# Kernel optimization log

Hardware: AMD Instinct MI355X
Metric: run time of the kernel (lower is better)

Reference implementation:

```python
import jax, jax.numpy as jnp
import numpy as np

N = 30000
SLOPE = 0.2  # PyG GATConv default negative_slope


def _gat_conv(x, src, dst, W, a_src, a_dst, b, heads, out_ch, concat):
    """PyG GATConv (add_self_loops already applied), eval mode (no dropout).
    x: [N, F_in]; src/dst: [E] int; W: [F_in, heads*out_ch];
    a_src/a_dst: [heads, out_ch]; b: [heads*out_ch] or [out_ch]."""
    n = x.shape[0]
    h = (x @ W).reshape(n, heads, out_ch)              # [N, H, C]
    al_src = jnp.sum(h * a_src, axis=-1)               # [N, H]
    al_dst = jnp.sum(h * a_dst, axis=-1)               # [N, H]
    e = jax.nn.leaky_relu(al_src[src] + al_dst[dst], SLOPE)  # [E, H]
    # segment softmax over incoming edges of each destination node
    m = jax.ops.segment_max(e, dst, num_segments=n)
    ex = jnp.exp(e - m[dst])
    denom = jax.ops.segment_sum(ex, dst, num_segments=n)
    alpha = ex / (denom[dst] + 1e-16)                  # [E, H]
    msg = h[src] * alpha[..., None]                    # [E, H, C]
    out = jax.ops.segment_sum(msg, dst, num_segments=n)  # [N, H, C]
    out = out.reshape(n, heads * out_ch) if concat else out.mean(axis=1)
    return out + b


def setup_inputs() -> dict:
    key = jax.random.key(0)
    ks = jax.random.split(key, 20)
    E = 480000
    IN, H0, H1, LAT = 256, 64, 128, 32
    HEADS = 4
    x = jax.random.normal(ks[0], (N, IN), dtype=jnp.float32)
    edge_index = jax.random.randint(ks[1], (2, E), 0, N, dtype=jnp.int32)

    def gp(k, fin, heads, outc, concat):
        k1, k2, k3, k4 = jax.random.split(k, 4)
        s = 0.1
        W = jax.random.normal(k1, (fin, heads * outc), dtype=jnp.float32) * s
        a_s = jax.random.normal(k2, (heads, outc), dtype=jnp.float32) * s
        a_d = jax.random.normal(k3, (heads, outc), dtype=jnp.float32) * s
        b = jax.random.normal(k4, (heads * outc if concat else outc,), dtype=jnp.float32) * s
        return W, a_s, a_d, b

    W1, as1, ad1, b1 = gp(ks[2], IN, HEADS, H0, True)
    W2, as2, ad2, b2 = gp(ks[3], H0 * HEADS, HEADS, H1, True)
    Wm, asm, adm, bm = gp(ks[4], H1 * HEADS, HEADS, LAT, False)
    Wl, asl, adl, bl = gp(ks[5], H1 * HEADS, HEADS, LAT, False)
    return dict(x=x, edge_index=edge_index,
                W1=W1, as1=as1, ad1=ad1, b1=b1,
                W2=W2, as2=as2, ad2=ad2, b2=b2,
                Wm=Wm, asm=asm, adm=adm, bm=bm,
                Wl=Wl, asl=asl, adl=adl, bl=bl)


def reference(x, edge_index, W1, as1, ad1, b1, W2, as2, ad2, b2,
              Wm, asm, adm, bm, Wl, asl, adl, bl):
    n = x.shape[0]
    # add self loops (PyG GATConv default)
    loop = jnp.arange(n, dtype=edge_index.dtype)
    src = jnp.concatenate([edge_index[0], loop])
    dst = jnp.concatenate([edge_index[1], loop])

    out = _gat_conv(x, src, dst, W1, as1, ad1, b1, heads=4, out_ch=64, concat=True)
    out = jax.nn.relu(out)
    out = _gat_conv(out, src, dst, W2, as2, ad2, b2, heads=4, out_ch=128, concat=True)
    out = jax.nn.relu(out)
    # F.dropout with training=False (eval) is identity
    z_mean = _gat_conv(out, src, dst, Wm, asm, adm, bm, heads=4, out_ch=32, concat=False)
    z_logstd = _gat_conv(out, src, dst, Wl, asl, adl, bl, heads=4, out_ch=32, concat=False)
    return z_mean, z_logstd
```

## Files before the change

### kernel.cpp

```cpp
#include <hip/hip_runtime.h>
#include <cstddef>

typedef __attribute__((ext_vector_type(8))) short short8;
typedef __attribute__((ext_vector_type(4))) float f32x4;
typedef __attribute__((ext_vector_type(8))) _Float16 half8;
typedef __attribute__((ext_vector_type(4))) _Float16 half4;

__device__ __forceinline__ unsigned short f2h(float f) {
    union { _Float16 h; unsigned short u; } x; x.h = (_Float16)f; return x.u;
}
__device__ __forceinline__ float lrelu(float v) { return v > 0.f ? v : 0.2f * v; }


__global__ void count_edges_kernel(const int* __restrict__ ei, int E, int N,
                                   int* __restrict__ cnt) {
    int e = blockIdx.x * blockDim.x + threadIdx.x;
    if (e >= E + N) return;
    int d = (e < E) ? ei[E + e] : (e - E);
    atomicAdd(&cnt[d], 1);
}

__global__ void scan_kernel(int* __restrict__ cnt, int* __restrict__ rp, int n) {
    __shared__ int sh[1024];
    int t = threadIdx.x;
    int chunk = (n + 1023) >> 10;
    int beg = t * chunk;
    int end = beg + chunk < n ? beg + chunk : n;
    int local = 0;
    for (int i = beg; i < end; i++) local += cnt[i];
    sh[t] = local;
    __syncthreads();
    for (int off = 1; off < 1024; off <<= 1) {
        int v = (t >= off) ? sh[t - off] : 0;
        __syncthreads();
        sh[t] += v;
        __syncthreads();
    }
    int run = (t == 0) ? 0 : sh[t - 1];
    for (int i = beg; i < end; i++) {
        int c = cnt[i];
        cnt[i] = 0;
        run += c;
        rp[i + 1] = run;
    }
    if (t == 0) rp[0] = 0;
}

__global__ void scatter_edges_kernel(const int* __restrict__ ei, int E, int N,
                                     const int* __restrict__ rp, int* __restrict__ cur,
                                     int* __restrict__ csrc) {
    int e = blockIdx.x * blockDim.x + threadIdx.x;
    if (e >= E + N) return;
    int s, d;
    if (e < E) { s = ei[e]; d = ei[E + e]; } else { s = e - E; d = s; }
    int pos = rp[d] + atomicAdd(&cur[d], 1);
    csrc[pos] = s;
}


__global__ void f32_to_f16_pad4_kernel(const float* __restrict__ in,
                                       unsigned short* __restrict__ out,
                                       int rows, int cols, int padRows) {
    int i = blockIdx.x * blockDim.x + threadIdx.x;
    int total = (padRows * cols) >> 2;
    if (i >= total) return;
    int r = (i * 4) / cols;
    ushort4 o;
    if (r < rows) {
        float4 v = *(const float4*)(in + (size_t)i * 4);
        o = make_ushort4(f2h(v.x), f2h(v.y), f2h(v.z), f2h(v.w));
    } else {
        o = make_ushort4(0, 0, 0, 0);
    }
    *(ushort4*)(out + (size_t)i * 4) = o;
}

__global__ void transpose_all_kernel(
    const float* __restrict__ W1, const float* __restrict__ W2,
    const float* __restrict__ Wm, const float* __restrict__ Wl,
    unsigned short* __restrict__ W1t, unsigned short* __restrict__ W2t,
    unsigned short* __restrict__ WmlT) {
    int i = blockIdx.x * blockDim.x + threadIdx.x;
    if (i < 65536) {
        int k = i >> 8, n = i & 255;
        W1t[(size_t)n * 256 + k] = f2h(W1[i]);
    } else if (i < 65536 + 131072) {
        int j = i - 65536;
        int k = j >> 9, n = j & 511;
        W2t[(size_t)n * 256 + k] = f2h(W2[j]);
    } else if (i < 65536 + 131072 + 65536) {
        int j = i - 196608;
        int k = j >> 7, n = j & 127;
        WmlT[(size_t)n * 512 + k] = f2h(Wm[j]);
    } else if (i < 65536 + 131072 + 131072) {
        int j = i - 262144;
        int k = j >> 7, n = j & 127;
        WmlT[(size_t)(128 + n) * 512 + k] = f2h(Wl[j]);
    }
}


__global__ __launch_bounds__(256) void gemm_f16_kernel(
    const unsigned short* __restrict__ A, const unsigned short* __restrict__ Bt,
    unsigned short* __restrict__ C, int M, int K, int Nc,
    float* __restrict__ al_s, float* __restrict__ al_d,
    const float* __restrict__ aslo, const float* __restrict__ adlo,
    const float* __restrict__ ashi, const float* __restrict__ adhi,
    int csplit, int Chead, int H) {
    __shared__ short As[64 * 32];
    __shared__ short Bs[128 * 32];
    __shared__ float salS[64][4];
    __shared__ float salD[64][4];
    int tid = threadIdx.x;
    int bm = blockIdx.y * 64;
    int bn = blockIdx.x * 128;
    int wave = tid >> 6, lane = tid & 63;
    int wm = (wave >> 1) * 32, wn = (wave & 1) * 64;
    int lm = lane & 15, lq = lane >> 4;

    f32x4 acc[2][4] = {};

    int c0 = tid, c1 = tid + 256;
    const unsigned short* Ap0 = A + (size_t)(bm + (c0 >> 2)) * K + (c0 & 3) * 8;
    const unsigned short* Bp0 = Bt + (size_t)(bn + (c0 >> 2)) * K + (c0 & 3) * 8;
    const unsigned short* Bp1 = Bt + (size_t)(bn + (c1 >> 2)) * K + (c1 & 3) * 8;

    short8 a0 = *(const short8*)(Ap0);
    short8 b0 = *(const short8*)(Bp0);
    short8 b1 = *(const short8*)(Bp1);

    for (int kk = 0; kk < K; kk += 32) {
        __syncthreads();
        *(short8*)&As[c0 * 8] = a0;
        *(short8*)&Bs[c0 * 8] = b0;
        *(short8*)&Bs[c1 * 8] = b1;
        if (kk + 32 < K) {
            a0 = *(const short8*)(Ap0 + kk + 32);
            b0 = *(const short8*)(Bp0 + kk + 32);
            b1 = *(const short8*)(Bp1 + kk + 32);
        }
        __syncthreads();
        half8 af[2], bf[4];
#pragma unroll
        for (int t = 0; t < 2; t++)
            af[t] = *(const half8*)&As[(wm + t * 16 + lm) * 32 + lq * 8];
#pragma unroll
        for (int t = 0; t < 4; t++)
            bf[t] = *(const half8*)&Bs[(wn + t * 16 + lm) * 32 + lq * 8];
#pragma unroll
        for (int tm = 0; tm < 2; tm++)
#pragma unroll
            for (int tn = 0; tn < 4; tn++)
                acc[tm][tn] = __builtin_amdgcn_mfma_f32_16x16x32_f16(
                    af[tm], bf[tn], acc[tm][tn], 0, 0, 0);
    }

#pragma unroll
    for (int tm = 0; tm < 2; tm++) {
#pragma unroll
        for (int r = 0; r < 4; r++) {
            int row = bm + wm + tm * 16 + lq * 4 + r;
            if (row < M) {
#pragma unroll
                for (int tn = 0; tn < 4; tn++) {
                    int col = bn + wn + tn * 16 + lm;
                    C[(size_t)row * Nc + col] = f2h(acc[tm][tn][r]);
                }
            }
        }
    }

    float asv[4], adv[4];
#pragma unroll
    for (int tn = 0; tn < 4; tn++) {
        int col = bn + wn + tn * 16 + lm;
        bool hi = col >= csplit;
        int cc = hi ? col - csplit : col;
        asv[tn] = hi ? ashi[cc] : aslo[cc];
        adv[tn] = hi ? adhi[cc] : adlo[cc];
    }
    int gb = wn >> 5;
#pragma unroll
    for (int tm = 0; tm < 2; tm++) {
#pragma unroll
        for (int r = 0; r < 4; r++) {
#pragma unroll
            for (int p = 0; p < 2; p++) {
                float s1 = acc[tm][2 * p][r] * asv[2 * p]
                         + acc[tm][2 * p + 1][r] * asv[2 * p + 1];
                float s2 = acc[tm][2 * p][r] * adv[2 * p]
                         + acc[tm][2 * p + 1][r] * adv[2 * p + 1];
#pragma unroll
                for (int off = 8; off >= 1; off >>= 1) {
                    s1 += __shfl_xor(s1, off);
                    s2 += __shfl_xor(s2, off);
                }
                if (lm == 0) {
                    int rl = wm + tm * 16 + lq * 4 + r;
                    salS[rl][gb + p] = s1;
                    salD[rl][gb + p] = s2;
                }
            }
        }
    }
    __syncthreads();
    if (tid < 64) {
        int row = bm + tid;
        if (row < M) {
            int hb = bn / Chead;
            int HB = 128 / Chead;
            int GH = Chead >> 5;
            for (int i = 0; i < HB; i++) {
                float ss = 0.f, sd = 0.f;
                for (int j = 0; j < GH; j++) {
                    ss += salS[tid][i * GH + j];
                    sd += salD[tid][i * GH + j];
                }
                al_s[(size_t)row * H + hb + i] = ss;
                al_d[(size_t)row * H + hb + i] = sd;
            }
        }
    }
}


template <int H4, int V, int MODE>
__global__ __launch_bounds__(256) void gat_fused_kernel(
    const int* __restrict__ rp, const int* __restrict__ csrc,
    const float* __restrict__ al_s, const float* __restrict__ al_d,
    const unsigned short* __restrict__ h,
    const float* __restrict__ bias1, const float* __restrict__ bias2,
    void* __restrict__ out1v, void* __restrict__ out2v, int HC, int C, int N) {
    const int H = 4 * H4;
    __shared__ int lds_src[4][64];
    __shared__ float lds_alpha[4][64 * 4 * H4];
    __shared__ float shred[4][256];
    int wv = threadIdx.x >> 6;
    int lane = threadIdx.x & 63;
    int n = blockIdx.x * 4 + wv;
    if (n >= N) return;
    int beg = rp[n], end = rp[n + 1];
    int deg = end - beg;

    float ad[H];
#pragma unroll
    for (int g = 0; g < H4; g++)
        *(float4*)&ad[g * 4] = *(const float4*)(al_d + (size_t)n * H + g * 4);

    int ch = lane * V;
    int hh = ch / C;
    half8 acc8 = {};
    half4 acc4 = {};

    if (deg <= 64) {
        bool act = lane < deg;
        int s = act ? csrc[beg + lane] : 0;
        float v[H], m[H], ex[H], sum[H];
#pragma unroll
        for (int g = 0; g < H4; g++) {
            float4 as = *(const float4*)(al_s + (size_t)s * H + g * 4);
            v[g * 4 + 0] = lrelu(as.x + ad[g * 4 + 0]);
            v[g * 4 + 1] = lrelu(as.y + ad[g * 4 + 1]);
            v[g * 4 + 2] = lrelu(as.z + ad[g * 4 + 2]);
            v[g * 4 + 3] = lrelu(as.w + ad[g * 4 + 3]);
        }
#pragma unroll
        for (int j = 0; j < H; j++) m[j] = act ? v[j] : -3.402823466e38f;
#pragma unroll
        for (int off = 32; off >= 1; off >>= 1)
#pragma unroll
            for (int j = 0; j < H; j++) m[j] = fmaxf(m[j], __shfl_xor(m[j], off));
#pragma unroll
        for (int j = 0; j < H; j++) {
            ex[j] = act ? __expf(v[j] - m[j]) : 0.f;
            sum[j] = ex[j];
        }
#pragma unroll
        for (int off = 32; off >= 1; off >>= 1)
#pragma unroll
            for (int j = 0; j < H; j++) sum[j] += __shfl_xor(sum[j], off);
        if (act) {
            lds_src[wv][lane] = s;
#pragma unroll
            for (int g = 0; g < H4; g++) {
                float4 o;
                o.x = ex[g * 4 + 0] / (sum[g * 4 + 0] + 1e-16f);
                o.y = ex[g * 4 + 1] / (sum[g * 4 + 1] + 1e-16f);
                o.z = ex[g * 4 + 2] / (sum[g * 4 + 2] + 1e-16f);
                o.w = ex[g * 4 + 3] / (sum[g * 4 + 3] + 1e-16f);
                *(float4*)&lds_alpha[wv][lane * H + g * 4] = o;
            }
        }
        int t = 0;
        for (; t + 8 <= deg; t += 8) {
            int ss[8]; float av[8];
#pragma unroll
            for (int u = 0; u < 8; u++) {
                ss[u] = lds_src[wv][t + u];
                av[u] = lds_alpha[wv][(t + u) * H + hh];
            }
            if constexpr (V == 8) {
                half8 hv[8];
#pragma unroll
                for (int u = 0; u < 8; u++)
                    hv[u] = *(const half8*)(h + (size_t)ss[u] * HC + ch);
#pragma unroll
                for (int u = 0; u < 8; u++) {
                    _Float16 ah = (_Float16)av[u];
                    half8 a2;
#pragma unroll
                    for (int i = 0; i < 8; i++) a2[i] = ah;
                    acc8 += hv[u] * a2;
                }
            } else {
                half4 hv[8];
#pragma unroll
                for (int u = 0; u < 8; u++)
                    hv[u] = *(const half4*)(h + (size_t)ss[u] * HC + ch);
#pragma unroll
                for (int u = 0; u < 8; u++) {
                    _Float16 ah = (_Float16)av[u];
                    half4 a2;
#pragma unroll
                    for (int i = 0; i < 4; i++) a2[i] = ah;
                    acc4 += hv[u] * a2;
                }
            }
        }
        for (; t < deg; t++) {
            int s2 = lds_src[wv][t];
            _Float16 ah = (_Float16)lds_alpha[wv][t * H + hh];
            if constexpr (V == 8) {
                half8 hv = *(const half8*)(h + (size_t)s2 * HC + ch);
                half8 a2;
#pragma unroll
                for (int i = 0; i < 8; i++) a2[i] = ah;
                acc8 += hv * a2;
            } else {
                half4 hv = *(const half4*)(h + (size_t)s2 * HC + ch);
                half4 a2;
#pragma unroll
                for (int i = 0; i < 4; i++) a2[i] = ah;
                acc4 += hv * a2;
            }
        }
    } else {
        float m[H], sum[H];
#pragma unroll
        for (int j = 0; j < H; j++) m[j] = -3.402823466e38f;
        for (int e = beg + lane; e < end; e += 64) {
            int s = csrc[e];
#pragma unroll
            for (int g = 0; g < H4; g++) {
                float4 as = *(const float4*)(al_s + (size_t)s * H + g * 4);
                m[g * 4 + 0] = fmaxf(m[g * 4 + 0], lrelu(as.x + ad[g * 4 + 0]));
                m[g * 4 + 1] = fmaxf(m[g * 4 + 1], lrelu(as.y + ad[g * 4 + 1]));
                m[g * 4 + 2] = fmaxf(m[g * 4 + 2], lrelu(as.z + ad[g * 4 + 2]));
                m[g * 4 + 3] = fmaxf(m[g * 4 + 3], lrelu(as.w + ad[g * 4 + 3]));
            }
        }
#pragma unroll
        for (int off = 32; off >= 1; off >>= 1)
#pragma unroll
            for (int j = 0; j < H; j++) m[j] = fmaxf(m[j], __shfl_xor(m[j], off));
#pragma unroll
        for (int j = 0; j < H; j++) sum[j] = 0.f;
        for (int e = beg + lane; e < end; e += 64) {
            int s = csrc[e];
#pragma unroll
            for (int g = 0; g < H4; g++) {
                float4 as = *(const float4*)(al_s + (size_t)s * H + g * 4);
                sum[g * 4 + 0] += __expf(lrelu(as.x + ad[g * 4 + 0]) - m[g * 4 + 0]);
                sum[g * 4 + 1] += __expf(lrelu(as.y + ad[g * 4 + 1]) - m[g * 4 + 1]);
                sum[g * 4 + 2] += __expf(lrelu(as.z + ad[g * 4 + 2]) - m[g * 4 + 2]);
                sum[g * 4 + 3] += __expf(lrelu(as.w + ad[g * 4 + 3]) - m[g * 4 + 3]);
            }
        }
#pragma unroll
        for (int off = 32; off >= 1; off >>= 1)
#pragma unroll
            for (int j = 0; j < H; j++) sum[j] += __shfl_xor(sum[j], off);
        float r[H];
#pragma unroll
        for (int j = 0; j < H; j++) r[j] = 1.0f / (sum[j] + 1e-16f);
        for (int base = beg; base < end; base += 64) {
            int cn = end - base < 64 ? end - base : 64;
            if (lane < cn) {
                int s = csrc[base + lane];
                lds_src[wv][lane] = s;
#pragma unroll
                for (int g = 0; g < H4; g++) {
                    float4 as = *(const float4*)(al_s + (size_t)s * H + g * 4);
                    float4 o;
                    o.x = __expf(lrelu(as.x + ad[g * 4 + 0]) - m[g * 4 + 0]) * r[g * 4 + 0];
                    o.y = __expf(lrelu(as.y + ad[g * 4 + 1]) - m[g * 4 + 1]) * r[g * 4 + 1];
                    o.z = __expf(lrelu(as.z + ad[g * 4 + 2]) - m[g * 4 + 2]) * r[g * 4 + 2];
                    o.w = __expf(lrelu(as.w + ad[g * 4 + 3]) - m[g * 4 + 3]) * r[g * 4 + 3];
                    *(float4*)&lds_alpha[wv][lane * H + g * 4] = o;
                }
            }
            for (int t = 0; t < cn; t++) {
                int s2 = lds_src[wv][t];
                _Float16 ah = (_Float16)lds_alpha[wv][t * H + hh];
                if constexpr (V == 8) {
                    half8 hv = *(const half8*)(h + (size_t)s2 * HC + ch);
                    half8 a2;
#pragma unroll
                    for (int i = 0; i < 8; i++) a2[i] = ah;
                    acc8 += hv * a2;
                } else {
                    half4 hv = *(const half4*)(h + (size_t)s2 * HC + ch);
                    half4 a2;
#pragma unroll
                    for (int i = 0; i < 4; i++) a2[i] = ah;
                    acc4 += hv * a2;
                }
            }
        }
    }

    float accf[V];
#pragma unroll
    for (int j = 0; j < V; j++)
        accf[j] = (V == 8) ? (float)acc8[j] : (float)acc4[j];

    if constexpr (MODE == 0) {
        unsigned short* out = (unsigned short*)out1v;
        unsigned short o[V];
#pragma unroll
        for (int j = 0; j < V; j++)
            o[j] = f2h(fmaxf(accf[j] + bias1[ch + j], 0.f));
        if constexpr (V == 8) {
            short8 ov;
#pragma unroll
            for (int j = 0; j < 8; j++) ov[j] = (short)o[j];
            *(short8*)(out + (size_t)n * HC + ch) = ov;
        } else {
            *(ushort4*)(out + (size_t)n * HC + ch) = make_ushort4(o[0], o[1], o[2], o[3]);
        }
    } else {
        *(float4*)&shred[wv][ch] = make_float4(accf[0], accf[1], accf[2], accf[3]);
        if (lane < 32) {
            float v1 = (shred[wv][lane] + shred[wv][lane + 32] + shred[wv][lane + 64]
                        + shred[wv][lane + 96]) * 0.25f + bias1[lane];
            float v2 = (shred[wv][lane + 128] + shred[wv][lane + 160]
                        + shred[wv][lane + 192] + shred[wv][lane + 224]) * 0.25f
                       + bias2[lane];
            ((float*)out1v)[(size_t)n * 32 + lane] = v1;
            ((float*)out2v)[(size_t)n * 32 + lane] = v2;
        }
    }
}


extern "C" void kernel_launch(void* const* d_in, const int* in_sizes, int n_in,
                              void* d_out, int out_size, void* d_ws, size_t ws_size,
                              hipStream_t stream) {
    (void)n_in; (void)out_size; (void)ws_size;
    const float* x   = (const float*)d_in[0];
    const int*   ei  = (const int*)d_in[1];
    const float* W1  = (const float*)d_in[2];
    const float* as1 = (const float*)d_in[3];
    const float* ad1 = (const float*)d_in[4];
    const float* b1  = (const float*)d_in[5];
    const float* W2  = (const float*)d_in[6];
    const float* as2 = (const float*)d_in[7];
    const float* ad2 = (const float*)d_in[8];
    const float* b2  = (const float*)d_in[9];
    const float* Wm  = (const float*)d_in[10];
    const float* a_sm = (const float*)d_in[11];
    const float* a_dm = (const float*)d_in[12];
    const float* bm  = (const float*)d_in[13];
    const float* Wl  = (const float*)d_in[14];
    const float* a_sl = (const float*)d_in[15];
    const float* a_dl = (const float*)d_in[16];
    const float* bl  = (const float*)d_in[17];
    float* outp = (float*)d_out;

    const int N  = in_sizes[0] / 256;
    const int E  = in_sizes[1] / 2;
    const int ET = E + N;
    const int gM128 = (N + 127) / 128;
    const int Mp = gM128 * 128;
    const int gM64 = (N + 63) / 64;

    auto align_up = [](size_t v) { return (v + 255) & ~(size_t)255; };
    char* w = (char*)d_ws;
    int* row_ptr = (int*)w;  w += align_up((size_t)(N + 1) * 4);
    int* cnt     = (int*)w;  w += align_up((size_t)N * 4);
    int* csrc    = (int*)w;  w += align_up((size_t)ET * 4);
    float* al_s  = (float*)w; w += align_up((size_t)N * 8 * 4);
    float* al_d  = (float*)w; w += align_up((size_t)N * 8 * 4);
    unsigned short* xb   = (unsigned short*)w; w += align_up((size_t)Mp * 256 * 2);
    unsigned short* W1t  = (unsigned short*)w; w += align_up((size_t)256 * 256 * 2);
    unsigned short* W2t  = (unsigned short*)w; w += align_up((size_t)512 * 256 * 2);
    unsigned short* WmlT = (unsigned short*)w; w += align_up((size_t)256 * 512 * 2);
    unsigned short* bufH = (unsigned short*)w; w += align_up((size_t)Mp * 512 * 2);
    unsigned short* bufO = (unsigned short*)w; w += align_up((size_t)Mp * 512 * 2);

    int gzE = (ET + 255) / 256;
    hipMemsetAsync(cnt, 0, (size_t)N * 4, stream);
    count_edges_kernel<<<gzE, 256, 0, stream>>>(ei, E, N, cnt);
    scan_kernel<<<1, 1024, 0, stream>>>(cnt, row_ptr, N);
    scatter_edges_kernel<<<gzE, 256, 0, stream>>>(ei, E, N, row_ptr, cnt, csrc);

    f32_to_f16_pad4_kernel<<<((Mp * 256 / 4) + 255) / 256, 256, 0, stream>>>(
        x, xb, N, 256, Mp);
    transpose_all_kernel<<<(393216 + 255) / 256, 256, 0, stream>>>(
        W1, W2, Wm, Wl, W1t, W2t, WmlT);

    int gF = (N + 3) / 4;

    gemm_f16_kernel<<<dim3(2, gM64), 256, 0, stream>>>(
        xb, W1t, bufH, N, 256, 256, al_s, al_d, as1, ad1, as1, ad1, 256, 64, 4);
    gat_fused_kernel<1, 4, 0><<<gF, 256, 0, stream>>>(
        row_ptr, csrc, al_s, al_d, bufH, b1, nullptr, bufO, nullptr, 256, 64, N);

    gemm_f16_kernel<<<dim3(4, gM64), 256, 0, stream>>>(
        bufO, W2t, bufH, N, 256, 512, al_s, al_d, as2, ad2, as2, ad2, 512, 128, 4);
    gat_fused_kernel<1, 8, 0><<<gF, 256, 0, stream>>>(
        row_ptr, csrc, al_s, al_d, bufH, b2, nullptr, bufO, nullptr, 512, 128, N);

    gemm_f16_kernel<<<dim3(2, gM64), 256, 0, stream>>>(
        bufO, WmlT, bufH, N, 512, 256, al_s, al_d, a_sm, a_dm, a_sl, a_dl, 128, 32, 8);
    gat_fused_kernel<2, 4, 1><<<gF, 256, 0, stream>>>(
        row_ptr, csrc, al_s, al_d, bufH, bm, bl, outp, outp + (size_t)N * 32, 256, 32, N);
}
```

Measured before the change: 444.1 us.

## Merge prep kernels and fuse edge counting into first GEMM launch

Result: slower. 516.7 us (+16.4%).

```diff
diff --git a/kernel.cpp b/kernel.cpp
--- a/kernel.cpp
+++ b/kernel.cpp
@@ -5,6 +5,7 @@
 typedef __attribute__((ext_vector_type(4))) float f32x4;
 typedef __attribute__((ext_vector_type(8))) _Float16 half8;
 typedef __attribute__((ext_vector_type(4))) _Float16 half4;
+typedef __attribute__((ext_vector_type(4))) unsigned short ushortx4;
 
 __device__ __forceinline__ unsigned short f2h(float f) {
     union { _Float16 h; unsigned short u; } x; x.h = (_Float16)f; return x.u;
@@ -12,13 +13,52 @@
 __device__ __forceinline__ float lrelu(float v) { return v > 0.f ? v : 0.2f * v; }
 
 
-__global__ void count_edges_kernel(const int* __restrict__ ei, int E, int N,
-                                   int* __restrict__ cnt) {
-    int e = blockIdx.x * blockDim.x + threadIdx.x;
-    if (e >= E + N) return;
-    int d = (e < E) ? ei[E + e] : (e - E);
-    atomicAdd(&cnt[d], 1);
-}
+__global__ void prep_kernel(const float* __restrict__ x, unsigned short* __restrict__ xb,
+                            int N, int Mp,
+                            const float* __restrict__ W1, const float* __restrict__ W2,
+                            const float* __restrict__ Wm, const float* __restrict__ Wl,
+                            unsigned short* __restrict__ W1t, unsigned short* __restrict__ W2t,
+                            unsigned short* __restrict__ WmlT,
+                            int* __restrict__ cnt, int nZero, int nConv) {
+    int b = blockIdx.x;
+    int tid = threadIdx.x;
+    if (b < nZero) {
+        int i = b * 256 + tid;
+        if (i < N) cnt[i] = 0;
+    } else if (b < nZero + nConv) {
+        int i = (b - nZero) * 256 + tid;
+        int total = (Mp * 256) >> 2;
+        if (i >= total) return;
+        int r = (i * 4) >> 8;
+        ushort4 o;
+        if (r < N) {
+            float4 v = *(const float4*)(x + (size_t)i * 4);
+            o = make_ushort4(f2h(v.x), f2h(v.y), f2h(v.z), f2h(v.w));
+        } else {
+            o = make_ushort4(0, 0, 0, 0);
+        }
+        *(ushort4*)(xb + (size_t)i * 4) = o;
+    } else {
+        int i = (b - nZero - nConv) * 256 + tid;
+        if (i < 65536) {
+            int k = i >> 8, n = i & 255;
+            W1t[(size_t)n * 256 + k] = f2h(W1[i]);
+        } else if (i < 65536 + 131072) {
+            int j = i - 65536;
+            int k = j >> 9, n = j & 511;
+            W2t[(size_t)n * 256 + k] = f2h(W2[j]);
+        } else if (i < 65536 + 131072 + 65536) {
+            int j = i - 196608;
+            int k = j >> 7, n = j & 127;
+            WmlT[(size_t)n * 512 + k] = f2h(Wm[j]);
+        } else if (i < 65536 + 131072 + 131072) {
+            int j = i - 262144;
+            int k = j >> 7, n = j & 127;
+            WmlT[(size_t)(128 + n) * 512 + k] = f2h(Wl[j]);
+        }
+    }
+}
+
 
 __global__ void scan_kernel(int* __restrict__ cnt, int* __restrict__ rp, int n) {
     __shared__ int sh[1024];
@@ -58,62 +98,20 @@
 }
 
 
-__global__ void f32_to_f16_pad4_kernel(const float* __restrict__ in,
-                                       unsigned short* __restrict__ out,
-                                       int rows, int cols, int padRows) {
-    int i = blockIdx.x * blockDim.x + threadIdx.x;
-    int total = (padRows * cols) >> 2;
-    if (i >= total) return;
-    int r = (i * 4) / cols;
-    ushort4 o;
-    if (r < rows) {
-        float4 v = *(const float4*)(in + (size_t)i * 4);
-        o = make_ushort4(f2h(v.x), f2h(v.y), f2h(v.z), f2h(v.w));
-    } else {
-        o = make_ushort4(0, 0, 0, 0);
-    }
-    *(ushort4*)(out + (size_t)i * 4) = o;
-}
-
-__global__ void transpose_all_kernel(
-    const float* __restrict__ W1, const float* __restrict__ W2,
-    const float* __restrict__ Wm, const float* __restrict__ Wl,
-    unsigned short* __restrict__ W1t, unsigned short* __restrict__ W2t,
-    unsigned short* __restrict__ WmlT) {
-    int i = blockIdx.x * blockDim.x + threadIdx.x;
-    if (i < 65536) {
-        int k = i >> 8, n = i & 255;
-        W1t[(size_t)n * 256 + k] = f2h(W1[i]);
-    } else if (i < 65536 + 131072) {
-        int j = i - 65536;
-        int k = j >> 9, n = j & 511;
-        W2t[(size_t)n * 256 + k] = f2h(W2[j]);
-    } else if (i < 65536 + 131072 + 65536) {
-        int j = i - 196608;
-        int k = j >> 7, n = j & 127;
-        WmlT[(size_t)n * 512 + k] = f2h(Wm[j]);
-    } else if (i < 65536 + 131072 + 131072) {
-        int j = i - 262144;
-        int k = j >> 7, n = j & 127;
-        WmlT[(size_t)(128 + n) * 512 + k] = f2h(Wl[j]);
-    }
-}
-
-
-__global__ __launch_bounds__(256) void gemm_f16_kernel(
+struct GemmSmem {
+    short As[64 * 32];
+    short Bs[128 * 32];
+    float salS[64][4];
+    float salD[64][4];
+};
+
+__device__ __forceinline__ void gemm_f16_tile(
     const unsigned short* __restrict__ A, const unsigned short* __restrict__ Bt,
     unsigned short* __restrict__ C, int M, int K, int Nc,
     float* __restrict__ al_s, float* __restrict__ al_d,
     const float* __restrict__ aslo, const float* __restrict__ adlo,
     const float* __restrict__ ashi, const float* __restrict__ adhi,
-    int csplit, int Chead, int H) {
-    __shared__ short As[64 * 32];
-    __shared__ short Bs[128 * 32];
-    __shared__ float salS[64][4];
-    __shared__ float salD[64][4];
-    int tid = threadIdx.x;
-    int bm = blockIdx.y * 64;
-    int bn = blockIdx.x * 128;
+    int csplit, int Chead, int H, GemmSmem& sm, int bm, int bn, int tid) {
     int wave = tid >> 6, lane = tid & 63;
     int wm = (wave >> 1) * 32, wn = (wave & 1) * 64;
     int lm = lane & 15, lq = lane >> 4;
@@ -131,9 +129,9 @@
 
     for (int kk = 0; kk < K; kk += 32) {
         __syncthreads();
-        *(short8*)&As[c0 * 8] = a0;
-        *(short8*)&Bs[c0 * 8] = b0;
-        *(short8*)&Bs[c1 * 8] = b1;
+        *(short8*)&sm.As[c0 * 8] = a0;
+        *(short8*)&sm.Bs[c0 * 8] = b0;
+        *(short8*)&sm.Bs[c1 * 8] = b1;
         if (kk + 32 < K) {
             a0 = *(const short8*)(Ap0 + kk + 32);
             b0 = *(const short8*)(Bp0 + kk + 32);
@@ -143,10 +141,10 @@
         half8 af[2], bf[4];
 #pragma unroll
         for (int t = 0; t < 2; t++)
-            af[t] = *(const half8*)&As[(wm + t * 16 + lm) * 32 + lq * 8];
+            af[t] = *(const half8*)&sm.As[(wm + t * 16 + lm) * 32 + lq * 8];
 #pragma unroll
         for (int t = 0; t < 4; t++)
-            bf[t] = *(const half8*)&Bs[(wn + t * 16 + lm) * 32 + lq * 8];
+            bf[t] = *(const half8*)&sm.Bs[(wn + t * 16 + lm) * 32 + lq * 8];
 #pragma unroll
         for (int tm = 0; tm < 2; tm++)
 #pragma unroll
@@ -197,8 +195,8 @@
                 }
                 if (lm == 0) {
                     int rl = wm + tm * 16 + lq * 4 + r;
-                    salS[rl][gb + p] = s1;
-                    salD[rl][gb + p] = s2;
+                    sm.salS[rl][gb + p] = s1;
+                    sm.salD[rl][gb + p] = s2;
                 }
             }
         }
@@ -213,12 +211,51 @@
             for (int i = 0; i < HB; i++) {
                 float ss = 0.f, sd = 0.f;
                 for (int j = 0; j < GH; j++) {
-                    ss += salS[tid][i * GH + j];
-                    sd += salD[tid][i * GH + j];
+                    ss += sm.salS[tid][i * GH + j];
+                    sd += sm.salD[tid][i * GH + j];
                 }
                 al_s[(size_t)row * H + hb + i] = ss;
                 al_d[(size_t)row * H + hb + i] = sd;
             }
+        }
+    }
+}
+
+__global__ __launch_bounds__(256) void gemm_f16_kernel(
+    const unsigned short* __restrict__ A, const unsigned short* __restrict__ Bt,
+    unsigned short* __restrict__ C, int M, int K, int Nc,
+    float* __restrict__ al_s, float* __restrict__ al_d,
+    const float* __restrict__ aslo, const float* __restrict__ adlo,
+    const float* __restrict__ ashi, const float* __restrict__ adhi,
+    int csplit, int Chead, int H, int nbx) {
+    __shared__ GemmSmem sm;
+    int b = blockIdx.x;
+    int bn = (b % nbx) * 128;
+    int bm = (b / nbx) * 64;
+    gemm_f16_tile(A, Bt, C, M, K, Nc, al_s, al_d, aslo, adlo, ashi, adhi,
+                  csplit, Chead, H, sm, bm, bn, threadIdx.x);
+}
+
+__global__ __launch_bounds__(256) void gemm1_count_kernel(
+    const unsigned short* __restrict__ A, const unsigned short* __restrict__ Bt,
+    unsigned short* __restrict__ C, int M, int K, int Nc,
+    float* __restrict__ al_s, float* __restrict__ al_d,
+    const float* __restrict__ aslo, const float* __restrict__ adlo,
+    const float* __restrict__ ashi, const float* __restrict__ adhi,
+    int csplit, int Chead, int H, int nbx, int nGemm,
+    const int* __restrict__ ei, int E, int N, int* __restrict__ cnt) {
+    __shared__ GemmSmem sm;
+    int b = blockIdx.x;
+    if (b < nGemm) {
+        int bn = (b % nbx) * 128;
+        int bm = (b / nbx) * 64;
+        gemm_f16_tile(A, Bt, C, M, K, Nc, al_s, al_d, aslo, adlo, ashi, adhi,
+                      csplit, Chead, H, sm, bm, bn, threadIdx.x);
+    } else {
+        int e = (b - nGemm) * 256 + threadIdx.x;
+        if (e < E + N) {
+            int d = (e < E) ? ei[E + e] : (e - E);
+            atomicAdd(&cnt[d], 1);
         }
     }
 }
@@ -434,9 +471,12 @@
             short8 ov;
 #pragma unroll
             for (int j = 0; j < 8; j++) ov[j] = (short)o[j];
-            *(short8*)(out + (size_t)n * HC + ch) = ov;
+            __builtin_nontemporal_store(ov, (short8*)(out + (size_t)n * HC + ch));
         } else {
-            *(ushort4*)(out + (size_t)n * HC + ch) = make_ushort4(o[0], o[1], o[2], o[3]);
+            ushortx4 ov;
+#pragma unroll
+            for (int j = 0; j < 4; j++) ov[j] = o[j];
+            __builtin_nontemporal_store(ov, (ushortx4*)(out + (size_t)n * HC + ch));
         }
     } else {
         *(float4*)&shred[wv][ch] = make_float4(accf[0], accf[1], accf[2], accf[3]);
@@ -446,8 +486,8 @@
             float v2 = (shred[wv][lane + 128] + shred[wv][lane + 160]
                         + shred[wv][lane + 192] + shred[wv][lane + 224]) * 0.25f
                        + bias2[lane];
-            ((float*)out1v)[(size_t)n * 32 + lane] = v1;
-            ((float*)out2v)[(size_t)n * 32 + lane] = v2;
+            __builtin_nontemporal_store(v1, (float*)out1v + (size_t)n * 32 + lane);
+            __builtin_nontemporal_store(v2, (float*)out2v + (size_t)n * 32 + lane);
         }
     }
 }
@@ -498,31 +538,33 @@
     unsigned short* bufH = (unsigned short*)w; w += align_up((size_t)Mp * 512 * 2);
     unsigned short* bufO = (unsigned short*)w; w += align_up((size_t)Mp * 512 * 2);
 
+    int nZero = (N + 255) / 256;
+    int nConv = (Mp * 256 / 4 + 255) / 256;
+    int nTrans = (393216 + 255) / 256;
+    prep_kernel<<<nZero + nConv + nTrans, 256, 0, stream>>>(
+        x, xb, N, Mp, W1, W2, Wm, Wl, W1t, W2t, WmlT, cnt, nZero, nConv);
+
     int gzE = (ET + 255) / 256;
-    hipMemsetAsync(cnt, 0, (size_t)N * 4, stream);
-    count_edges_kernel<<<gzE, 256, 0, stream>>>(ei, E, N, cnt);
+    int gF = (N + 3) / 4;
+
+    int nGemm1 = 2 * gM64;
+    gemm1_count_kernel<<<nGemm1 + gzE, 256, 0, stream>>>(
+        xb, W1t, bufH, N, 256, 256, al_s, al_d, as1, ad1, as1, ad1, 256, 64, 4,
+        2, nGemm1, ei, E, N, cnt);
+
     scan_kernel<<<1, 1024, 0, stream>>>(cnt, row_ptr, N);
     scatter_edges_kernel<<<gzE, 256, 0, stream>>>(ei, E, N, row_ptr, cnt, csrc);
 
-    f32_to_f16_pad4_kernel<<<((Mp * 256 / 4) + 255) / 256, 256, 0, stream>>>(
-        x, xb, N, 256, Mp);
-    transpose_all_kernel<<<(393216 + 255) / 256, 256, 0, stream>>>(
-        W1, W2, Wm, Wl, W1t, W2t, WmlT);
-
-    int gF = (N + 3) / 4;
-
-    gemm_f16_kernel<<<dim3(2, gM64), 256, 0, stream>>>(
-        xb, W1t, bufH, N, 256, 256, al_s, al_d, as1, ad1, as1, ad1, 256, 64, 4);
     gat_fused_kernel<1, 4, 0><<<gF, 256, 0, stream>>>(
         row_ptr, csrc, al_s, al_d, bufH, b1, nullptr, bufO, nullptr, 256, 64, N);
 
-    gemm_f16_kernel<<<dim3(4, gM64), 256, 0, stream>>>(
-        bufO, W2t, bufH, N, 256, 512, al_s, al_d, as2, ad2, as2, ad2, 512, 128, 4);
+    gemm_f16_kernel<<<4 * gM64, 256, 0, stream>>>(
+        bufO, W2t, bufH, N, 256, 512, al_s, al_d, as2, ad2, as2, ad2, 512, 128, 4, 4);
     gat_fused_kernel<1, 8, 0><<<gF, 256, 0, stream>>>(
         row_ptr, csrc, al_s, al_d, bufH, b2, nullptr, bufO, nullptr, 512, 128, N);
 
-    gemm_f16_kernel<<<dim3(2, gM64), 256, 0, stream>>>(
-        bufO, WmlT, bufH, N, 512, 256, al_s, al_d, a_sm, a_dm, a_sl, a_dl, 128, 32, 8);
+    gemm_f16_kernel<<<2 * gM64, 256, 0, stream>>>(
+        bufO, WmlT, bufH, N, 512, 256, al_s, al_d, a_sm, a_dm, a_sl, a_dl, 128, 32, 8, 2);
     gat_fused_kernel<2, 4, 1><<<gF, 256, 0, stream>>>(
         row_ptr, csrc, al_s, al_d, bufH, bm, bl, outp, outp + (size_t)N * 32, 256, 32, N);
 }
```
